# Kernel optimization log

Measured on AMD Instinct MI355X. Metric: run time of the kernel, lower is better.

## Reference

```python
import jax, jax.numpy as jnp
import numpy as np

D_MODEL = 2048
NUM_HEADS = 16
D_K = D_MODEL // NUM_HEADS  # 128
THETA = 10000.0
BATCH = 2
SEQ = 2048


def _rope(v, pos):
    # v: [..., S, d_k], pos: [..., S] int
    half = v.shape[-1] // 2
    inv_freq = THETA ** (-(jnp.arange(half, dtype=jnp.float32) * 2.0) / v.shape[-1])
    ang = pos[..., None].astype(jnp.float32) * inv_freq  # [..., S, half]
    cos, sin = jnp.cos(ang), jnp.sin(ang)
    x1 = v[..., 0::2]
    x2 = v[..., 1::2]
    r1 = x1 * cos - x2 * sin
    r2 = x1 * sin + x2 * cos
    return jnp.stack([r1, r2], axis=-1).reshape(v.shape)


def setup_inputs() -> dict:
    key = jax.random.key(0)
    ks = jax.random.split(key, 5)
    scale = D_MODEL ** -0.5
    x = jax.random.normal(ks[0], (BATCH, SEQ, D_MODEL), dtype=jnp.float32)
    WQ = jax.random.normal(ks[1], (D_MODEL, D_MODEL), dtype=jnp.float32) * scale
    WK = jax.random.normal(ks[2], (D_MODEL, D_MODEL), dtype=jnp.float32) * scale
    WV = jax.random.normal(ks[3], (D_MODEL, D_MODEL), dtype=jnp.float32) * scale
    WO = jax.random.normal(ks[4], (D_MODEL, D_MODEL), dtype=jnp.float32) * scale
    token_positions = jnp.broadcast_to(jnp.arange(SEQ, dtype=jnp.int32), (BATCH, SEQ))
    return {"x": x, "token_positions": token_positions, "WQ": WQ, "WK": WK, "WV": WV, "WO": WO}


def reference(x, token_positions, WQ, WK, WV, WO):
    B, S, _ = x.shape
    split = lambda t: t.reshape(B, S, NUM_HEADS, D_K).transpose(0, 2, 1, 3)  # [B,H,S,d]
    Q = split(x @ WQ.T)
    K = split(x @ WK.T)
    V = split(x @ WV.T)
    pos = token_positions[:, None, :]  # broadcast over heads
    Q = _rope(Q, pos)
    K = _rope(K, pos)
    scores = jnp.einsum('bhqd,bhkd->bhqk', Q, K) / np.sqrt(D_K).astype(np.float32)
    causal = jnp.arange(S)[:, None] >= jnp.arange(S)[None, :]  # [S,S]
    scores = jnp.where(causal, scores, -jnp.inf)
    attn = jax.nn.softmax(scores, axis=-1)
    out = jnp.einsum('bhqk,bhkd->bhqd', attn, V)
    out = out.transpose(0, 2, 1, 3).reshape(B, S, D_MODEL)
    return out @ WO.T
```

## Files before the change

kernel.cpp:

```cpp
#include <hip/hip_runtime.h>

typedef unsigned short ushort;
typedef __attribute__((ext_vector_type(8))) __bf16 bf16x8;
typedef __attribute__((ext_vector_type(8))) ushort ushort8;
typedef __attribute__((ext_vector_type(4))) float f32x4;
typedef __attribute__((ext_vector_type(16))) float f32x16;
typedef __attribute__((ext_vector_type(4))) unsigned u32x4;

#define DM 2048
#define NH 16
#define DK 128
#define BATCH 2
#define SEQ 2048
#define MROWS (BATCH*SEQ)

#define GLDS16(g, l) __builtin_amdgcn_global_load_lds(                         \
    (const __attribute__((address_space(1))) void*)(g),                        \
    (__attribute__((address_space(3))) void*)(l), 16, 0, 0)

__device__ __forceinline__ ushort f2bf(float f) {
  unsigned u = __builtin_bit_cast(unsigned, f);
  u += 0x7fffu + ((u >> 16) & 1u);
  return (ushort)(u >> 16);
}

__device__ __forceinline__ unsigned cvtpk(float lo, float hi) {
  unsigned r;
  asm("v_cvt_pk_bf16_f32 %0, %1, %2" : "=v"(r) : "v"(lo), "v"(hi));
  return r;
}

__device__ __forceinline__ void pswap(unsigned& a, unsigned& b) {
#if __has_builtin(__builtin_amdgcn_permlane32_swap)
  auto r = __builtin_amdgcn_permlane32_swap(a, b, false, false);
  a = r[0];
  b = r[1];
#else
  unsigned as = (unsigned)__shfl_xor((int)a, 32), bs = (unsigned)__shfl_xor((int)b, 32);
  bool hi = (threadIdx.x & 32) != 0;
  unsigned na = hi ? bs : a;
  unsigned nb = hi ? b : as;
  a = na;
  b = nb;
#endif
}

__global__ __launch_bounds__(256) void cvt_all(const float* __restrict__ x,
                                               const float* __restrict__ w0,
                                               const float* __restrict__ w1,
                                               const float* __restrict__ w2,
                                               const float* __restrict__ w3,
                                               ushort* __restrict__ xb,
                                               ushort* __restrict__ o0,
                                               ushort* __restrict__ o1,
                                               ushort* __restrict__ o2,
                                               ushort* __restrict__ o3) {
  int b = blockIdx.x;
  const float* src;
  ushort* dst;
  int lb;
  if (b < 4096) { src = x; dst = xb; lb = b; }
  else {
    int wsel = (b - 4096) >> 11;
    lb = (b - 4096) & 2047;
    src = (wsel == 0) ? w0 : (wsel == 1) ? w1 : (wsel == 2) ? w2 : w3;
    dst = (wsel == 0) ? o0 : (wsel == 1) ? o1 : (wsel == 2) ? o2 : o3;
  }
  int i = lb * 256 + threadIdx.x;
  const float4* p = (const float4*)src;
  float4 a = p[2 * i], bq = p[2 * i + 1];
  ushort8 o;
  o[0] = f2bf(a.x); o[1] = f2bf(a.y); o[2] = f2bf(a.z); o[3] = f2bf(a.w);
  o[4] = f2bf(bq.x); o[5] = f2bf(bq.y); o[6] = f2bf(bq.z); o[7] = f2bf(bq.w);
  *(ushort8*)(dst + (size_t)8 * i) = o;
}

__global__ __launch_bounds__(512, 2) void gemmF_qkv(const ushort* __restrict__ A,
                                                    const ushort* __restrict__ W0,
                                                    const ushort* __restrict__ W1,
                                                    const ushort* __restrict__ W2,
                                                    ushort* __restrict__ Qo,
                                                    ushort* __restrict__ Ko,
                                                    ushort* __restrict__ Vt,
                                                    const int* __restrict__ tpos) {
  extern __shared__ ushort lds[];
  constexpr int NT = DM / 64;
  constexpr int BUFSZ = 8192 + 24576;
  int f = ((int)blockIdx.x & 7) * 64 + ((int)blockIdx.x >> 3);
  int row0 = (f >> 4) * 128, col0 = (f & 15) * 128;
  const ushort* Bw[3] = {W0, W1, W2};
  const int tid = threadIdx.x;
  const int wid = tid >> 6, lane = tid & 63;
  const int l15 = lane & 15, lhi = lane >> 4;
  const int wm = wid >> 2, wn = wid & 3;
  const int swz = l15 & 7;

  f32x4 acc[4][6];
  const f32x4 z4 = {0.f, 0.f, 0.f, 0.f};
#pragma unroll
  for (int mq = 0; mq < 4; ++mq)
#pragma unroll
    for (int i = 0; i < 6; ++i) acc[mq][i] = z4;

  auto stage = [&](int kt, int buf) {
    ushort* dstA = &lds[buf * BUFSZ];
    const ushort* srcA = A + (size_t)row0 * DM + kt * 64;
#pragma unroll
    for (int j = 0; j < 2; ++j) {
      int g = j * 512 + tid;
      int r = g >> 3, c = g & 7;
      GLDS16(srcA + (size_t)r * DM + ((c ^ (r & 7)) * 8),
             &dstA[(j * 512 + wid * 64) * 8]);
    }
#pragma unroll
    for (int w3 = 0; w3 < 3; ++w3) {
      ushort* dstB = &lds[buf * BUFSZ + 8192 + w3 * 8192];
      const ushort* srcB = Bw[w3] + (size_t)col0 * DM + kt * 64;
#pragma unroll
      for (int j = 0; j < 2; ++j) {
        int g = j * 512 + tid;
        int r = g >> 3, c = g & 7;
        GLDS16(srcB + (size_t)r * DM + ((c ^ (r & 7)) * 8),
               &dstB[(j * 512 + wid * 64) * 8]);
      }
    }
  };

  stage(0, 0);
  asm volatile("s_waitcnt vmcnt(0)" ::: "memory");
  asm volatile("s_barrier" ::: "memory");

  for (int t = 0; t < NT; ++t) {
    const int cb = t & 1;
    const ushort* Ab = &lds[cb * BUFSZ];
    const ushort* Bb = Ab + 8192;
    if (t + 1 < NT) stage(t + 1, cb ^ 1);
#pragma unroll
    for (int ks = 0; ks < 2; ++ks) {
      bf16x8 af[4];
#pragma unroll
      for (int mq = 0; mq < 4; ++mq) {
        int row = wm * 64 + mq * 16 + l15;
        af[mq] = *(const bf16x8*)&Ab[row * 64 + (((ks * 4 + lhi) ^ swz) * 8)];
      }
      bf16x8 bfr[6];
#pragma unroll
      for (int w3 = 0; w3 < 3; ++w3)
#pragma unroll
        for (int n = 0; n < 2; ++n) {
          int row = wn * 32 + n * 16 + l15;
          bfr[w3 * 2 + n] =
              *(const bf16x8*)&Bb[w3 * 8192 + row * 64 + (((ks * 4 + lhi) ^ swz) * 8)];
        }
      __builtin_amdgcn_s_setprio(1);
#pragma unroll
      for (int mq = 0; mq < 4; ++mq)
#pragma unroll
        for (int i = 0; i < 6; ++i)
          acc[mq][i] = __builtin_amdgcn_mfma_f32_16x16x32_bf16(af[mq], bfr[i], acc[mq][i], 0, 0, 0);
      __builtin_amdgcn_s_setprio(0);
    }
    asm volatile("s_waitcnt vmcnt(0)" ::: "memory");
    asm volatile("s_barrier" ::: "memory");
  }

  int posr[4][4];
#pragma unroll
  for (int mq = 0; mq < 4; ++mq) {
    int grow = row0 + wm * 64 + mq * 16 + lhi * 4;
#pragma unroll
    for (int j = 0; j < 4; ++j) {
      int r = grow + j;
      posr[mq][j] = tpos[(r >> 11) * SEQ + (r & (SEQ - 1))];
    }
  }
#pragma unroll
  for (int mq = 0; mq < 4; ++mq) {
    int grow = row0 + wm * 64 + mq * 16 + lhi * 4;
#pragma unroll
    for (int n = 0; n < 2; ++n) {
      int gcol = col0 + wn * 32 + n * 16 + l15;
      int h = gcol >> 7, d = gcol & (DK - 1);
      float freq = exp2f(-0.20762050593045976f * (float)(d >> 1));
      bool oddl = (d & 1) != 0;
      float sn[4], cs[4];
#pragma unroll
      for (int j = 0; j < 4; ++j) {
        float ang = (float)posr[mq][j] * freq;
        sn[j] = __sinf(ang);
        cs[j] = __cosf(ang);
      }
#pragma unroll
      for (int w3 = 0; w3 < 2; ++w3) {
        ushort* Ow = w3 ? Ko : Qo;
#pragma unroll
        for (int j = 0; j < 4; ++j) {
          int r = grow + j;
          float v = acc[mq][w3 * 2 + n][j];
          float vp = __shfl_xor(v, 1);
          float outv = oddl ? (vp * sn[j] + v * cs[j]) : (v * cs[j] - vp * sn[j]);
          int b = r >> 11, s = r & (SEQ - 1);
          Ow[((size_t)(b * NH + h) * SEQ + s) * DK + d] = f2bf(outv);
        }
      }
    }
  }

  {
    ushort* lv = &lds[0];
#pragma unroll
    for (int mq = 0; mq < 4; ++mq)
#pragma unroll
      for (int n = 0; n < 2; ++n) {
        int col = wn * 32 + n * 16 + l15;
#pragma unroll
        for (int j = 0; j < 4; ++j) {
          int rowl = wm * 64 + mq * 16 + lhi * 4 + j;
          lv[rowl * 136 + col] = f2bf(acc[mq][4 + n][j]);
        }
      }
    __syncthreads();
    int b = row0 >> 11, s0r = row0 & (SEQ - 1), h = col0 >> 7;
    ushort* vtbase = Vt + (size_t)(b * NH + h) * DK * SEQ;
#pragma unroll
    for (int cc = 0; cc < 4; ++cc) {
      int c = cc * 512 + tid;
      int d = c >> 4, sc = (c & 15) * 8;
      ushort8 o;
#pragma unroll
      for (int k = 0; k < 8; ++k) o[k] = lv[(sc + k) * 136 + d];
      *(ushort8*)&vtbase[(size_t)d * SEQ + s0r + sc] = o;
    }
  }
}

__global__ __launch_bounds__(512, 2) void gemmF_out(const ushort* __restrict__ A,
                                                    const ushort* __restrict__ Bm,
                                                    float* __restrict__ ofp) {
  extern __shared__ ushort lds[];
  constexpr int NT = DM / 64;
  constexpr int BUFSZ = 8192 + 16384;
  int xcd = (int)blockIdx.x & 7, bi = (int)blockIdx.x >> 3;
  int row0 = (((xcd >> 1) << 3) + (bi >> 2)) * 128;
  int col0 = (((xcd & 1) << 2) + (bi & 3)) * 256;
  const int tid = threadIdx.x;
  const int wid = tid >> 6, lane = tid & 63;
  const int l15 = lane & 15, lhi = lane >> 4;
  const int wm = wid >> 2, wn = wid & 3;
  const int swz = l15 & 7;

  f32x4 acc[4][4];
  const f32x4 z4 = {0.f, 0.f, 0.f, 0.f};
#pragma unroll
  for (int mq = 0; mq < 4; ++mq)
#pragma unroll
    for (int i = 0; i < 4; ++i) acc[mq][i] = z4;

  auto stage = [&](int kt, int buf) {
    ushort* dstA = &lds[buf * BUFSZ];
    const ushort* srcA = A + (size_t)row0 * DM + kt * 64;
#pragma unroll
    for (int j = 0; j < 2; ++j) {
      int g = j * 512 + tid;
      int r = g >> 3, c = g & 7;
      GLDS16(srcA + (size_t)r * DM + ((c ^ (r & 7)) * 8),
             &dstA[(j * 512 + wid * 64) * 8]);
    }
    ushort* dstB = &lds[buf * BUFSZ + 8192];
    const ushort* srcB = Bm + (size_t)col0 * DM + kt * 64;
#pragma unroll
    for (int j = 0; j < 4; ++j) {
      int g = j * 512 + tid;
      int r = g >> 3, c = g & 7;
      GLDS16(srcB + (size_t)r * DM + ((c ^ (r & 7)) * 8),
             &dstB[(j * 512 + wid * 64) * 8]);
    }
  };

  stage(0, 0);
  stage(1, 1);

  for (int t = 0; t < NT; ++t) {
    if (t + 1 < NT)
      asm volatile("s_waitcnt vmcnt(6)" ::: "memory");
    else
      asm volatile("s_waitcnt vmcnt(0)" ::: "memory");
    __builtin_amdgcn_s_barrier();

    const int cb = t & 1;
    const ushort* Ab = &lds[cb * BUFSZ];
    const ushort* Bb = Ab + 8192;
#pragma unroll
    for (int ks = 0; ks < 2; ++ks) {
      bf16x8 af[4];
#pragma unroll
      for (int mq = 0; mq < 4; ++mq) {
        int row = wm * 64 + mq * 16 + l15;
        af[mq] = *(const bf16x8*)&Ab[row * 64 + (((ks * 4 + lhi) ^ swz) * 8)];
      }
      bf16x8 bfr[4];
#pragma unroll
      for (int n = 0; n < 4; ++n) {
        int row = wn * 64 + n * 16 + l15;
        bfr[n] = *(const bf16x8*)&Bb[row * 64 + (((ks * 4 + lhi) ^ swz) * 8)];
      }
      __builtin_amdgcn_s_setprio(1);
#pragma unroll
      for (int mq = 0; mq < 4; ++mq)
#pragma unroll
        for (int n = 0; n < 4; ++n)
          acc[mq][n] = __builtin_amdgcn_mfma_f32_16x16x32_bf16(af[mq], bfr[n], acc[mq][n], 0, 0, 0);
      __builtin_amdgcn_s_setprio(0);
    }

    __builtin_amdgcn_s_barrier();
    if (t + 2 < NT) stage(t + 2, cb);
  }

#pragma unroll
  for (int mq = 0; mq < 4; ++mq) {
    int grow = row0 + wm * 64 + mq * 16 + lhi * 4;
#pragma unroll
    for (int n = 0; n < 4; ++n) {
      int gcol = col0 + wn * 64 + n * 16 + l15;
#pragma unroll
      for (int j = 0; j < 4; ++j)
        ofp[(size_t)(grow + j) * DM + gcol] = acc[mq][n][j];
    }
  }
}

__global__ __launch_bounds__(256, 2) void attn_kernel(const ushort* __restrict__ Qb,
                                                      const ushort* __restrict__ Kb,
                                                      const ushort* __restrict__ Vt,
                                                      ushort* __restrict__ attnb) {
  __shared__ ushort lds[32768];
  const int bx = blockIdx.x;
  const int u = bx & 255, hg = bx >> 8;
  const int qt = hg ? (15 - (u & 15)) : (u & 15);
  const int bh = (u >> 4) + hg * 16;
  const int tid = threadIdx.x;
  const int w = tid >> 6, lane = tid & 63;
  const int l31 = lane & 31, hi = lane >> 5;
  const int qb = qt * 128;
  const int qsb = qb + w * 32;
  const int q = qsb + l31;
  const size_t qk_base = (size_t)bh * SEQ * DK;
  const size_t v_base = (size_t)bh * DK * SEQ;
  const int nt = (qb + 128) >> 6;

  bf16x8 qf[8];
#pragma unroll
  for (int ks = 0; ks < 8; ++ks)
    qf[ks] = *(const bf16x8*)&Qb[qk_base + (size_t)q * DK + ks * 16 + hi * 8];

  f32x16 acc[4];
#pragma unroll
  for (int dt = 0; dt < 4; ++dt)
#pragma unroll
    for (int r = 0; r < 16; ++r) acc[dt][r] = 0.f;

  float m2 = -INFINITY, lsum = 0.f;
  const float cs2 = 0.08838834764831845f * 1.4426950408889634f;

  auto stage = [&](int t, int bufsel) {
    const int kb0 = t * 64;
#pragma unroll
    for (int i = 0; i < 4; ++i) {
      int g = w * 256 + i * 64 + lane;
      int row = g >> 4, c16 = g & 15;
      GLDS16(Kb + qk_base + (size_t)(kb0 + row) * DK + ((c16 ^ (row & 7)) * 8),
             &lds[bufsel * 8192 + (w * 256 + i * 64) * 8]);
    }
#pragma unroll
    for (int i = 0; i < 4; ++i) {
      int g = w * 256 + i * 64 + lane;
      int row = g >> 3, c8 = g & 7;
      GLDS16(Vt + v_base + (size_t)row * SEQ + kb0 + ((c8 ^ (row & 7)) * 8),
             &lds[16384 + bufsel * 8192 + (w * 256 + i * 64) * 8]);
    }
  };

  stage(0, 0);
  __syncthreads();
  int buf = 0;

  for (int t = 0; t < nt; ++t) {
    if (t + 1 < nt) stage(t + 1, buf ^ 1);
    const int kb0 = t * 64;
    if (kb0 <= qsb) {
      const ushort* lk = &lds[buf * 8192];
      const ushort* lv = &lds[16384 + buf * 8192];
      const int kb1 = kb0 + 32;
      const bool diag0 = (kb0 == qsb);
      const bool have1 = (kb1 <= qsb);
      const bool diag1 = (kb1 == qsb);
      const int sw = l31 & 7;

      f32x16 s0, s1;
#pragma unroll
      for (int r = 0; r < 16; ++r) { s0[r] = 0.f; s1[r] = 0.f; }
      __builtin_amdgcn_s_setprio(1);
#pragma unroll
      for (int ks = 0; ks < 8; ++ks) {
        int g = 2 * ks + hi;
        bf16x8 kf = *(const bf16x8*)&lk[(l31 * 16 + (g ^ sw)) * 8];
        s0 = __builtin_amdgcn_mfma_f32_32x32x16_bf16(kf, qf[ks], s0, 0, 0, 0);
      }
      if (have1) {
#pragma unroll
        for (int ks = 0; ks < 8; ++ks) {
          int g = 2 * ks + hi;
          bf16x8 kf = *(const bf16x8*)&lk[((32 + l31) * 16 + (g ^ sw)) * 8];
          s1 = __builtin_amdgcn_mfma_f32_32x32x16_bf16(kf, qf[ks], s1, 0, 0, 0);
        }
      }
      __builtin_amdgcn_s_setprio(0);

      float mx = -INFINITY;
#pragma unroll
      for (int r = 0; r < 16; ++r) {
        float v = s0[r] * cs2;
        if (diag0) {
          int kk = kb0 + (r & 3) + 8 * (r >> 2) + 4 * hi;
          if (kk > q) v = -INFINITY;
        }
        s0[r] = v;
        mx = fmaxf(mx, v);
      }
      if (have1) {
#pragma unroll
        for (int r = 0; r < 16; ++r) {
          float v = s1[r] * cs2;
          if (diag1) {
            int kk = kb1 + (r & 3) + 8 * (r >> 2) + 4 * hi;
            if (kk > q) v = -INFINITY;
          }
          s1[r] = v;
          mx = fmaxf(mx, v);
        }
      }
      {
        unsigned ma = __builtin_bit_cast(unsigned, mx), mb = ma;
        pswap(ma, mb);
        mx = fmaxf(__builtin_bit_cast(float, ma), __builtin_bit_cast(float, mb));
      }

      float sc = 1.f;
      if (!__all(mx <= m2 + 11.5f)) {
        float mnew = fmaxf(m2, mx);
        sc = exp2f(m2 - mnew);
        m2 = mnew;
#pragma unroll
        for (int dt = 0; dt < 4; ++dt)
#pragma unroll
          for (int r = 0; r < 16; ++r) acc[dt][r] *= sc;
      }
      float rs = 0.f;
#pragma unroll
      for (int r = 0; r < 16; ++r) {
        float p = exp2f(s0[r] - m2);
        s0[r] = p;
        rs += p;
      }
      if (have1) {
#pragma unroll
        for (int r = 0; r < 16; ++r) {
          float p = exp2f(s1[r] - m2);
          s1[r] = p;
          rs += p;
        }
      }
      {
        unsigned ra = __builtin_bit_cast(unsigned, rs), rb = ra;
        pswap(ra, rb);
        rs = __builtin_bit_cast(float, ra) + __builtin_bit_cast(float, rb);
      }
      lsum = lsum * sc + rs;

      unsigned w0[8];
#pragma unroll
      for (int i = 0; i < 8; ++i) w0[i] = cvtpk(s0[2 * i], s0[2 * i + 1]);
      pswap(w0[0], w0[2]); pswap(w0[1], w0[3]);
      pswap(w0[4], w0[6]); pswap(w0[5], w0[7]);
      u32x4 b00 = {w0[0], w0[1], w0[2], w0[3]};
      u32x4 b01 = {w0[4], w0[5], w0[6], w0[7]};
      bf16x8 pb00 = __builtin_bit_cast(bf16x8, b00);
      bf16x8 pb01 = __builtin_bit_cast(bf16x8, b01);
      bf16x8 pb10, pb11;
      if (have1) {
        unsigned w1[8];
#pragma unroll
        for (int i = 0; i < 8; ++i) w1[i] = cvtpk(s1[2 * i], s1[2 * i + 1]);
        pswap(w1[0], w1[2]); pswap(w1[1], w1[3]);
        pswap(w1[4], w1[6]); pswap(w1[5], w1[7]);
        u32x4 b10 = {w1[0], w1[1], w1[2], w1[3]};
        u32x4 b11 = {w1[4], w1[5], w1[6], w1[7]};
        pb10 = __builtin_bit_cast(bf16x8, b10);
        pb11 = __builtin_bit_cast(bf16x8, b11);
      }

      __builtin_amdgcn_s_setprio(1);
#pragma unroll
      for (int dt = 0; dt < 4; ++dt) {
        int vr = (dt * 32 + l31) * 8;
        bf16x8 vf0 = *(const bf16x8*)&lv[(vr + ((0 + hi) ^ sw)) * 8];
        bf16x8 vf1 = *(const bf16x8*)&lv[(vr + ((2 + hi) ^ sw)) * 8];
        acc[dt] = __builtin_amdgcn_mfma_f32_32x32x16_bf16(vf0, pb00, acc[dt], 0, 0, 0);
        acc[dt] = __builtin_amdgcn_mfma_f32_32x32x16_bf16(vf1, pb01, acc[dt], 0, 0, 0);
        if (have1) {
          bf16x8 vf2 = *(const bf16x8*)&lv[(vr + ((4 + hi) ^ sw)) * 8];
          bf16x8 vf3 = *(const bf16x8*)&lv[(vr + ((6 + hi) ^ sw)) * 8];
          acc[dt] = __builtin_amdgcn_mfma_f32_32x32x16_bf16(vf2, pb10, acc[dt], 0, 0, 0);
          acc[dt] = __builtin_amdgcn_mfma_f32_32x32x16_bf16(vf3, pb11, acc[dt], 0, 0, 0);
        }
      }
      __builtin_amdgcn_s_setprio(0);
    }
    __syncthreads();
    buf ^= 1;
  }

  ushort* eo = &lds[w * 32 * 136];
  float inv = 1.0f / lsum;
#pragma unroll
  for (int dt = 0; dt < 4; ++dt)
#pragma unroll
    for (int rq = 0; rq < 4; ++rq) {
      unsigned lo = cvtpk(acc[dt][4 * rq] * inv, acc[dt][4 * rq + 1] * inv);
      unsigned hh = cvtpk(acc[dt][4 * rq + 2] * inv, acc[dt][4 * rq + 3] * inv);
      uint2 pr; pr.x = lo; pr.y = hh;
      *(uint2*)&eo[l31 * 136 + dt * 32 + rq * 8 + hi * 4] = pr;
    }
  const int b = bh >> 4, h = bh & (NH - 1);
#pragma unroll
  for (int it = 0; it < 8; ++it) {
    int row = it * 4 + (lane >> 4);
    int c8 = (lane & 15) * 8;
    ushort8 v = *(const ushort8*)&eo[row * 136 + c8];
    *(ushort8*)&attnb[((size_t)b * SEQ + qsb + row) * DM + h * DK + c8] = v;
  }
}

extern "C" void kernel_launch(void* const* d_in, const int* in_sizes, int n_in,
                              void* d_out, int out_size, void* d_ws, size_t ws_size,
                              hipStream_t stream) {
  const float* x = (const float*)d_in[0];
  const int* tpos = (const int*)d_in[1];
  const float* WQ = (const float*)d_in[2];
  const float* WK = (const float*)d_in[3];
  const float* WV = (const float*)d_in[4];
  const float* WO = (const float*)d_in[5];
  float* out = (float*)d_out;
  char* ws = (char*)d_ws;

  ushort* xb  = (ushort*)(ws + 0);
  ushort* wqb = (ushort*)(ws + 16777216);
  ushort* wkb = (ushort*)(ws + 25165824);
  ushort* wvb = (ushort*)(ws + 33554432);
  ushort* wob = (ushort*)(ws + 41943040);
  ushort* Qb  = (ushort*)(ws + 50331648);
  ushort* Kb  = (ushort*)(ws + 67108864);
  ushort* Vt  = (ushort*)(ws + 83886080);
  ushort* attnb = (ushort*)(ws + 16777216);

  hipFuncSetAttribute(reinterpret_cast<const void*>(gemmF_qkv),
                      hipFuncAttributeMaxDynamicSharedMemorySize, 131072);
  hipFuncSetAttribute(reinterpret_cast<const void*>(gemmF_out),
                      hipFuncAttributeMaxDynamicSharedMemorySize, 98304);

  cvt_all<<<12288, 256, 0, stream>>>(x, WQ, WK, WV, WO, xb, wqb, wkb, wvb, wob);

  gemmF_qkv<<<512, 512, 131072, stream>>>(xb, wqb, wkb, wvb, Qb, Kb, Vt, tpos);

  attn_kernel<<<dim3(512), 256, 0, stream>>>(Qb, Kb, Vt, attnb);

  gemmF_out<<<256, 512, 98304, stream>>>(attnb, wob, out);
}
```

Baseline: 237.5 us.

## Rewrite QKV GEMM mainloop as 4-stage K=32 pipeline with split staging

```diff
diff --git a/kernel.cpp b/kernel.cpp
--- a/kernel.cpp
+++ b/kernel.cpp
@@ -75,7 +75,7 @@
   *(ushort8*)(dst + (size_t)8 * i) = o;
 }
 
-__global__ __launch_bounds__(512, 2) void gemmF_qkv(const ushort* __restrict__ A,
+__global__ __launch_bounds__(512, 2) void gemmP_qkv(const ushort* __restrict__ A,
                                                     const ushort* __restrict__ W0,
                                                     const ushort* __restrict__ W1,
                                                     const ushort* __restrict__ W2,
@@ -84,16 +84,15 @@
                                                     ushort* __restrict__ Vt,
                                                     const int* __restrict__ tpos) {
   extern __shared__ ushort lds[];
-  constexpr int NT = DM / 64;
-  constexpr int BUFSZ = 8192 + 24576;
-  int f = ((int)blockIdx.x & 7) * 64 + ((int)blockIdx.x >> 3);
-  int row0 = (f >> 4) * 128, col0 = (f & 15) * 128;
+  constexpr int NKH = DM / 32;
+  int xcd = (int)blockIdx.x & 7, bi = (int)blockIdx.x >> 3;
+  int row0 = (((xcd >> 2) << 4) + (bi >> 2)) * 128;
+  int col0 = (((xcd & 3) << 2) + (bi & 3)) * 128;
   const ushort* Bw[3] = {W0, W1, W2};
   const int tid = threadIdx.x;
   const int wid = tid >> 6, lane = tid & 63;
   const int l15 = lane & 15, lhi = lane >> 4;
   const int wm = wid >> 2, wn = wid & 3;
-  const int swz = l15 & 7;
 
   f32x4 acc[4][6];
   const f32x4 z4 = {0.f, 0.f, 0.f, 0.f};
@@ -102,66 +101,78 @@
 #pragma unroll
     for (int i = 0; i < 6; ++i) acc[mq][i] = z4;
 
-  auto stage = [&](int kt, int buf) {
-    ushort* dstA = &lds[buf * BUFSZ];
-    const ushort* srcA = A + (size_t)row0 * DM + kt * 64;
-#pragma unroll
-    for (int j = 0; j < 2; ++j) {
-      int g = j * 512 + tid;
-      int r = g >> 3, c = g & 7;
-      GLDS16(srcA + (size_t)r * DM + ((c ^ (r & 7)) * 8),
-             &dstA[(j * 512 + wid * 64) * 8]);
-    }
-#pragma unroll
-    for (int w3 = 0; w3 < 3; ++w3) {
-      ushort* dstB = &lds[buf * BUFSZ + 8192 + w3 * 8192];
-      const ushort* srcB = Bw[w3] + (size_t)col0 * DM + kt * 64;
-#pragma unroll
-      for (int j = 0; j < 2; ++j) {
-        int g = j * 512 + tid;
-        int r = g >> 3, c = g & 7;
-        GLDS16(srcB + (size_t)r * DM + ((c ^ (r & 7)) * 8),
-               &dstB[(j * 512 + wid * 64) * 8]);
-      }
-    }
+  const int srow = tid >> 2, sc4 = tid & 3;
+  const int ssw = (srow >> 1) & 3;
+  const ushort* srcA0 = A + (size_t)(row0 + srow) * DM + (sc4 ^ ssw) * 8;
+  const ushort* srcB0[3];
+#pragma unroll
+  for (int j = 0; j < 3; ++j)
+    srcB0[j] = Bw[j] + (size_t)(col0 + srow) * DM + (sc4 ^ ssw) * 8;
+
+  auto stageA = [&](int kh) {
+    GLDS16(srcA0 + kh * 32, &lds[(kh & 3) * 16384 + wid * 512]);
   };
-
-  stage(0, 0);
-  asm volatile("s_waitcnt vmcnt(0)" ::: "memory");
-  asm volatile("s_barrier" ::: "memory");
-
-  for (int t = 0; t < NT; ++t) {
-    const int cb = t & 1;
-    const ushort* Ab = &lds[cb * BUFSZ];
-    const ushort* Bb = Ab + 8192;
-    if (t + 1 < NT) stage(t + 1, cb ^ 1);
-#pragma unroll
-    for (int ks = 0; ks < 2; ++ks) {
-      bf16x8 af[4];
-#pragma unroll
-      for (int mq = 0; mq < 4; ++mq) {
-        int row = wm * 64 + mq * 16 + l15;
-        af[mq] = *(const bf16x8*)&Ab[row * 64 + (((ks * 4 + lhi) ^ swz) * 8)];
-      }
-      bf16x8 bfr[6];
-#pragma unroll
-      for (int w3 = 0; w3 < 3; ++w3)
-#pragma unroll
-        for (int n = 0; n < 2; ++n) {
-          int row = wn * 32 + n * 16 + l15;
-          bfr[w3 * 2 + n] =
-              *(const bf16x8*)&Bb[w3 * 8192 + row * 64 + (((ks * 4 + lhi) ^ swz) * 8)];
-        }
-      __builtin_amdgcn_s_setprio(1);
-#pragma unroll
-      for (int mq = 0; mq < 4; ++mq)
-#pragma unroll
-        for (int i = 0; i < 6; ++i)
-          acc[mq][i] = __builtin_amdgcn_mfma_f32_16x16x32_bf16(af[mq], bfr[i], acc[mq][i], 0, 0, 0);
-      __builtin_amdgcn_s_setprio(0);
-    }
-    asm volatile("s_waitcnt vmcnt(0)" ::: "memory");
-    asm volatile("s_barrier" ::: "memory");
+  auto stageB = [&](int kh) {
+    const int base = (kh & 3) * 16384 + 4096;
+#pragma unroll
+    for (int j = 0; j < 3; ++j)
+      GLDS16(srcB0[j] + kh * 32, &lds[base + j * 4096 + wid * 512]);
+  };
+
+  int aoff[4], boff[6];
+#pragma unroll
+  for (int m = 0; m < 4; ++m) {
+    int row = wm * 64 + m * 16 + l15;
+    aoff[m] = row * 32 + (lhi ^ ((row >> 1) & 3)) * 8;
+  }
+#pragma unroll
+  for (int w3 = 0; w3 < 3; ++w3)
+#pragma unroll
+    for (int n = 0; n < 2; ++n) {
+      int row = wn * 32 + n * 16 + l15;
+      boff[w3 * 2 + n] = 4096 + w3 * 4096 + row * 32 + (lhi ^ ((row >> 1) & 3)) * 8;
+    }
+
+  stageA(0); stageB(0);
+  stageA(1); stageB(1);
+  stageA(2); stageB(2);
+  asm volatile("s_waitcnt vmcnt(8)" ::: "memory");
+  __builtin_amdgcn_s_barrier();
+
+  for (int kh = 0; kh < NKH; ++kh) {
+    const int sb = (kh & 3) * 16384;
+    bf16x8 af0 = *(const bf16x8*)&lds[sb + aoff[0]];
+    bf16x8 af1 = *(const bf16x8*)&lds[sb + aoff[1]];
+    bf16x8 bfr[6];
+#pragma unroll
+    for (int i = 0; i < 6; ++i) bfr[i] = *(const bf16x8*)&lds[sb + boff[i]];
+    if (kh + 3 < NKH) stageA(kh + 3);
+    __builtin_amdgcn_s_barrier();
+    __builtin_amdgcn_s_setprio(1);
+#pragma unroll
+    for (int i = 0; i < 6; ++i) {
+      acc[0][i] = __builtin_amdgcn_mfma_f32_16x16x32_bf16(af0, bfr[i], acc[0][i], 0, 0, 0);
+      acc[1][i] = __builtin_amdgcn_mfma_f32_16x16x32_bf16(af1, bfr[i], acc[1][i], 0, 0, 0);
+    }
+    __builtin_amdgcn_s_setprio(0);
+    bf16x8 af2 = *(const bf16x8*)&lds[sb + aoff[2]];
+    bf16x8 af3 = *(const bf16x8*)&lds[sb + aoff[3]];
+    if (kh + 3 < NKH) stageB(kh + 3);
+    __builtin_amdgcn_s_barrier();
+    __builtin_amdgcn_s_setprio(1);
+#pragma unroll
+    for (int i = 0; i < 6; ++i) {
+      acc[2][i] = __builtin_amdgcn_mfma_f32_16x16x32_bf16(af2, bfr[i], acc[2][i], 0, 0, 0);
+      acc[3][i] = __builtin_amdgcn_mfma_f32_16x16x32_bf16(af3, bfr[i], acc[3][i], 0, 0, 0);
+    }
+    __builtin_amdgcn_s_setprio(0);
+    if (kh < NKH - 3)
+      asm volatile("s_waitcnt vmcnt(8)" ::: "memory");
+    else if (kh == NKH - 3)
+      asm volatile("s_waitcnt vmcnt(4)" ::: "memory");
+    else if (kh == NKH - 2)
+      asm volatile("s_waitcnt vmcnt(0)" ::: "memory");
+    __builtin_amdgcn_s_barrier();
   }
 
   int posr[4][4];
@@ -216,7 +227,7 @@
 #pragma unroll
         for (int j = 0; j < 4; ++j) {
           int rowl = wm * 64 + mq * 16 + lhi * 4 + j;
-          lv[rowl * 136 + col] = f2bf(acc[mq][4 + n][j]);
+          lv[rowl * 137 + col] = f2bf(acc[mq][4 + n][j]);
         }
       }
     __syncthreads();
@@ -228,7 +239,7 @@
       int d = c >> 4, sc = (c & 15) * 8;
       ushort8 o;
 #pragma unroll
-      for (int k = 0; k < 8; ++k) o[k] = lv[(sc + k) * 136 + d];
+      for (int k = 0; k < 8; ++k) o[k] = lv[(sc + k) * 137 + d];
       *(ushort8*)&vtbase[(size_t)d * SEQ + s0r + sc] = o;
     }
   }
@@ -564,14 +575,14 @@
   ushort* Vt  = (ushort*)(ws + 83886080);
   ushort* attnb = (ushort*)(ws + 16777216);
 
-  hipFuncSetAttribute(reinterpret_cast<const void*>(gemmF_qkv),
+  hipFuncSetAttribute(reinterpret_cast<const void*>(gemmP_qkv),
                       hipFuncAttributeMaxDynamicSharedMemorySize, 131072);
   hipFuncSetAttribute(reinterpret_cast<const void*>(gemmF_out),
                       hipFuncAttributeMaxDynamicSharedMemorySize, 98304);
 
   cvt_all<<<12288, 256, 0, stream>>>(x, WQ, WK, WV, WO, xb, wqb, wkb, wvb, wob);
 
-  gemmF_qkv<<<512, 512, 131072, stream>>>(xb, wqb, wkb, wvb, Qb, Kb, Vt, tpos);
+  gemmP_qkv<<<512, 512, 131072, stream>>>(xb, wqb, wkb, wvb, Qb, Kb, Vt, tpos);
 
   attn_kernel<<<dim3(512), 256, 0, stream>>>(Qb, Kb, Vt, attnb);
 
```

Measured after the change: 239.7 us. No clear change (+0.9%).
